# Performance work log

Measured on AMD Instinct MI355X. Metric: run time of the kernel, lower is better.

The kernel has to match this reference:

```python
import jax, jax.numpy as jnp
import numpy as np

N = 100000      # nodes
E = 1600000     # edges (before self-loops)
D = 14          # node_dim
H = 64          # hidden_dim
HEADS = 2
C = H // HEADS  # per-head channels = 32
NEG_SLOPE = 0.2 # GATv2Conv default


def setup_inputs() -> dict:
    key = jax.random.key(0)
    ks = jax.random.split(key, 32)
    p = lambda k, shape, s=0.05: (jax.random.normal(k, shape, jnp.float32) * s)
    inp = {
        'node_features': jax.random.normal(ks[0], (N, D), jnp.float32),
        'edge_index': jax.random.randint(ks[1], (2, E), 0, N, jnp.int32),
        # node_proj
        'proj_W': p(ks[2], (D, H)), 'proj_b': p(ks[3], (H,)),
        # GATv2 layer 1 (W_l for source msgs, W_r for target query)
        'g1_Wl': p(ks[4], (H, H)), 'g1_Wr': p(ks[5], (H, H)),
        'g1_att': p(ks[6], (HEADS, C)), 'g1_b': p(ks[7], (H,)),
        # GATv2 layer 2
        'g2_Wl': p(ks[8], (H, H)), 'g2_Wr': p(ks[9], (H, H)),
        'g2_att': p(ks[10], (HEADS, C)), 'g2_b': p(ks[11], (H,)),
        # LayerNorms
        'ln1_g': jnp.ones((H,), jnp.float32), 'ln1_b': jnp.zeros((H,), jnp.float32),
        'ln2_g': jnp.ones((H,), jnp.float32), 'ln2_b': jnp.zeros((H,), jnp.float32),
        # GRU (single step, h0=0). Gate order r,z,n like torch.
        'gru_Wi': p(ks[12], (H, 3 * H)), 'gru_Wh': p(ks[13], (H, 3 * H)),
        'gru_bi': p(ks[14], (3 * H,)), 'gru_bh': p(ks[15], (3 * H,)),
        # heads
        'hu_W': p(ks[16], (H, 1)), 'hu_b': p(ks[17], (1,)),
        'hf_W': p(ks[18], (H, 1)), 'hf_b': p(ks[19], (1,)),
        'ho_W': p(ks[20], (H, 1)), 'ho_b': p(ks[21], (1,)),
        'hc_W': p(ks[22], (H, 1)), 'hc_b': p(ks[23], (1,)),
    }
    return inp


def _layer_norm(x, g, b, eps=1e-5):
    mu = jnp.mean(x, axis=-1, keepdims=True)
    var = jnp.var(x, axis=-1, keepdims=True)
    return (x - mu) * jax.lax.rsqrt(var + eps) * g + b


def _gatv2(x, src, dst, Wl, Wr, att, b):
    n = x.shape[0]
    xl = (x @ Wl).reshape(n, HEADS, C)   # source messages
    xr = (x @ Wr).reshape(n, HEADS, C)   # target queries
    e = jax.nn.leaky_relu(xl[src] + xr[dst], NEG_SLOPE)       # [E', HEADS, C]
    s = jnp.einsum('ehc,hc->eh', e, att)                       # [E', HEADS]
    m = jax.ops.segment_max(s, dst, num_segments=n)            # segment softmax
    ex = jnp.exp(s - m[dst])
    den = jax.ops.segment_sum(ex, dst, num_segments=n)
    alpha = ex / (den[dst] + 1e-16)
    out = jax.ops.segment_sum(alpha[:, :, None] * xl[src], dst, num_segments=n)
    return out.reshape(n, H) + b


def reference(node_features, edge_index, proj_W, proj_b,
              g1_Wl, g1_Wr, g1_att, g1_b,
              g2_Wl, g2_Wr, g2_att, g2_b,
              ln1_g, ln1_b, ln2_g, ln2_b,
              gru_Wi, gru_Wh, gru_bi, gru_bh,
              hu_W, hu_b, hf_W, hf_b, ho_W, ho_b, hc_W, hc_b):
    n = node_features.shape[0]
    # add self-loops (PyG GATv2Conv default)
    loops = jnp.arange(n, dtype=edge_index.dtype)
    src = jnp.concatenate([edge_index[0], loops])
    dst = jnp.concatenate([edge_index[1], loops])

    x = node_features @ proj_W + proj_b
    x = jax.nn.elu(_gatv2(x, src, dst, g1_Wl, g1_Wr, g1_att, g1_b))
    x = _layer_norm(x, ln1_g, ln1_b)
    x = jax.nn.elu(_gatv2(x, src, dst, g2_Wl, g2_Wr, g2_att, g2_b))
    x = _layer_norm(x, ln2_g, ln2_b)

    # single-step GRU, h0 = 0 (gate order r, z, n as in torch)
    gi = x @ gru_Wi + gru_bi
    gi_r, gi_z, gi_n = jnp.split(gi, 3, axis=-1)
    bh_r, bh_z, bh_n = jnp.split(gru_bh, 3)
    r = jax.nn.sigmoid(gi_r + bh_r)
    z = jax.nn.sigmoid(gi_z + bh_z)
    nn_ = jnp.tanh(gi_n + r * bh_n)
    x = (1.0 - z) * nn_  # h' = (1-z)*n + z*h0, h0=0

    utilisation = jax.nn.sigmoid(x @ hu_W + hu_b)
    feasibility = jax.nn.sigmoid(x @ hf_W + hf_b)
    overtime = jax.nn.relu(x @ ho_W + ho_b)
    confidence = jax.nn.sigmoid(x @ hc_W + hc_b)
    return (utilisation, feasibility, overtime, confidence)
```

## Files before the change

### kernel.cpp

```cpp
#include <hip/hip_runtime.h>

#define NDIM 14
#define HDIM 64
#define NB 512
#define EPB 16
#define GSTR 72

typedef __attribute__((ext_vector_type(8))) _Float16 half8;
typedef __attribute__((ext_vector_type(2))) __fp16 fp16x2;
typedef __attribute__((ext_vector_type(4))) float f32x4;

static __device__ __forceinline__ float sigmoidf_(float x) { return 1.f / (1.f + __expf(-x)); }
static __device__ __forceinline__ float lrelu_(float x) { return x > 0.f ? x : 0.2f * x; }

static __device__ __forceinline__ float readlane_f(float x, int lane) {
  return __int_as_float(__builtin_amdgcn_readlane(__float_as_int(x), lane));
}

template <int CTRL>
static __device__ __forceinline__ float dpp_add_f(float x) {
  int v = __builtin_amdgcn_update_dpp(0, __float_as_int(x), CTRL, 0xF, 0xF, true);
  return x + __int_as_float(v);
}

static __device__ __forceinline__ float reduce16(float p) {
  p = dpp_add_f<0xB1>(p);
  p = dpp_add_f<0x4E>(p);
  p = dpp_add_f<0x141>(p);
  p = dpp_add_f<0x140>(p);
  return p;
}
static __device__ __forceinline__ float head_reduce32(float p) {
  p = reduce16(p);
  p += __int_as_float(__builtin_amdgcn_ds_swizzle(__float_as_int(p), 0x401F));
  return p;
}
static __device__ __forceinline__ float full_reduce64(float p) {
  p = head_reduce32(p);
  p += __shfl_xor(p, 32, 64);
  return p;
}

static __device__ __forceinline__ unsigned pk_add(unsigned a, unsigned b) {
  unsigned d; asm("v_pk_add_f16 %0, %1, %2" : "=v"(d) : "v"(a), "v"(b)); return d;
}
static __device__ __forceinline__ unsigned pk_mul(unsigned a, unsigned b) {
  unsigned d; asm("v_pk_mul_f16 %0, %1, %2" : "=v"(d) : "v"(a), "v"(b)); return d;
}
static __device__ __forceinline__ unsigned pk_max(unsigned a, unsigned b) {
  unsigned d; asm("v_pk_max_f16 %0, %1, %2" : "=v"(d) : "v"(a), "v"(b)); return d;
}
static __device__ __forceinline__ unsigned cvt_pk_u(float a, float b) {
  fp16x2 h = __builtin_amdgcn_cvt_pkrtz(a, b);
  unsigned u; __builtin_memcpy(&u, &h, 4); return u;
}
static __device__ __forceinline__ fp16x2 as_h2(unsigned u) {
  fp16x2 h; __builtin_memcpy(&h, &u, 4); return h;
}
static __device__ __forceinline__ float cvt_lo(unsigned u) {
  float r; asm("v_cvt_f32_f16 %0, %1" : "=v"(r) : "v"(u)); return r;
}
template <int CTRL>
static __device__ __forceinline__ unsigned pk_dpp_add(unsigned x) {
  unsigned v = (unsigned)__builtin_amdgcn_update_dpp(0, (int)x, CTRL, 0xF, 0xF, true);
  return pk_add(x, v);
}
static __device__ __forceinline__ unsigned pk_reduce32(unsigned p) {
  p = pk_dpp_add<0xB1>(p);
  p = pk_dpp_add<0x4E>(p);
  p = pk_dpp_add<0x141>(p);
  p = pk_dpp_add<0x140>(p);
  p = pk_add(p, (unsigned)__builtin_amdgcn_ds_swizzle((int)p, 0x401F));
  return p;
}

__global__ void k_binit(int* __restrict__ bcur, int cap) {
  int i = blockIdx.x * blockDim.x + threadIdx.x;
  if (i < NB) bcur[i] = i * cap;
}

__global__ void __launch_bounds__(256) k_bin(const int* __restrict__ ei,
                      long long* __restrict__ pairs, int* __restrict__ bucket_cur,
                      int E, int bsh) {
  __shared__ int h[NB];
  __shared__ int gb[NB];
  int t = threadIdx.x;
  for (int i = t; i < NB; i += 256) h[i] = 0;
  __syncthreads();
  int c0 = blockIdx.x * (256 * EPB);
  long long pr[EPB];
  int br[EPB];
#pragma unroll
  for (int i = 0; i < EPB; ++i) {
    int e = c0 + t + i * 256;
    if (e < E) {
      int s = ei[e], d = ei[E + e];
      int b = d >> bsh;
      int r = atomicAdd(&h[b], 1);
      pr[i] = ((long long)d << 32) | (unsigned)s;
      br[i] = b | (r << 9);
    } else br[i] = -1;
  }
  __syncthreads();
  for (int i = t; i < NB; i += 256)
    if (h[i]) gb[i] = atomicAdd(&bucket_cur[i], h[i]);
  __syncthreads();
#pragma unroll
  for (int i = 0; i < EPB; ++i) {
    if (br[i] >= 0) pairs[gb[br[i] & (NB - 1)] + (br[i] >> 9)] = pr[i];
  }
}

__global__ void __launch_bounds__(256) k_csr(const long long* __restrict__ pairs,
                      const int* __restrict__ bcur_final, int* __restrict__ row_off,
                      int* __restrict__ deg, int* __restrict__ csr_src,
                      int N, int bsh, int cap) {
  __shared__ int h[1024];
  __shared__ int cu[1024];
  __shared__ int wtot[4];
  int b = blockIdx.x;
  int node0 = b << bsh;
  int range = 1 << bsh;
  int nr = N - node0; if (nr > range) nr = range;
  if (nr <= 0) return;
  int e0 = b * cap, e1 = bcur_final[b];
  int tid = threadIdx.x;
  for (int i = tid; i < range; i += 256) h[i] = 0;
  __syncthreads();
  for (int e = e0 + tid; e < e1; e += 256)
    atomicAdd(&h[(int)(pairs[e] >> 32) - node0], 1);
  __syncthreads();
  if (range == 256) {
    int lane = tid & 63, wid = tid >> 6;
    int v = (tid < nr) ? h[tid] : 0;
    int x = v;
#pragma unroll
    for (int m = 1; m <= 32; m <<= 1) {
      int t2 = __shfl_up(x, m, 64);
      if (lane >= m) x += t2;
    }
    if (lane == 63) wtot[wid] = x;
    __syncthreads();
    int woff = 0;
#pragma unroll
    for (int w = 0; w < 4; ++w) woff += (w < wid) ? wtot[w] : 0;
    int excl = woff + x - v;
    if (tid < nr) {
      row_off[node0 + tid] = e0 + excl;
      deg[node0 + tid] = v;
      cu[tid] = excl;
    }
  } else {
    if (tid == 0) {
      int acc = 0;
      for (int i = 0; i < nr; ++i) {
        row_off[node0 + i] = e0 + acc;
        deg[node0 + i] = h[i];
        cu[i] = acc;
        acc += h[i];
      }
    }
  }
  __syncthreads();
  for (int e = e0 + tid; e < e1; e += 256) {
    long long pk = pairs[e];
    int d = (int)(pk >> 32), s = (int)pk;
    int p = atomicAdd(&cu[d - node0], 1);
    csr_src[e0 + p] = s;
  }
}

__global__ void k_wprep(const float* __restrict__ projW, const float* __restrict__ projB,
                        const float* __restrict__ Wl1, const float* __restrict__ Wr1,
                        const float* __restrict__ Wi, const float* __restrict__ Wl2,
                        const float* __restrict__ Wr2,
                        float* __restrict__ Wfl, float* __restrict__ Wfr,
                        float* __restrict__ bfl, float* __restrict__ bfr,
                        _Float16* __restrict__ Wt, _Float16* __restrict__ Wb) {
  int blk = blockIdx.x;
  if (blk < 4) {
    int t = blk * 256 + threadIdx.x;
    int total = (NDIM + 1) * HDIM;
    if (t >= total) return;
    int r = t / HDIM, c = t % HDIM;
    float al = 0.f, ar = 0.f;
    if (r < NDIM) {
      for (int k = 0; k < HDIM; ++k) {
        float w = projW[r * HDIM + k];
        al += w * Wl1[k * HDIM + c];
        ar += w * Wr1[k * HDIM + c];
      }
      Wfl[r * HDIM + c] = al;
      Wfr[r * HDIM + c] = ar;
    } else {
      for (int k = 0; k < HDIM; ++k) {
        float w = projB[k];
        al += w * Wl1[k * HDIM + c];
        ar += w * Wr1[k * HDIM + c];
      }
      bfl[c] = al;
      bfr[c] = ar;
    }
  } else if (blk < 52) {
    int t = (blk - 4) * 256 + threadIdx.x;
    if (t >= 192 * 64) return;
    int col = t / 64, row = t % 64;
    Wt[col * GSTR + row] = (_Float16)Wi[row * 192 + col];
  } else {
    int t = (blk - 52) * 256 + threadIdx.x;
    if (t >= 128 * 64) return;
    int col = t >> 6, row = t & 63;
    float v = (col < 64) ? Wl2[row * 64 + col] : Wr2[row * 64 + (col - 64)];
    Wb[col * GSTR + row] = (_Float16)v;
  }
}

__global__ void k1_xlxr(const float* __restrict__ nf, const float* __restrict__ Wfl,
                        const float* __restrict__ Wfr, const float* __restrict__ bfl,
                        const float* __restrict__ bfr, _Float16* __restrict__ XL16,
                        float* __restrict__ XR, int N) {
  int n = blockIdx.x * (blockDim.x >> 6) + (threadIdx.x >> 6);
  int j = threadIdx.x & 63;
  if (n >= N) return;
  float nfv = (j < NDIM) ? nf[n * NDIM + j] : 0.f;
  float al = bfl[j], ar = bfr[j];
#pragma unroll
  for (int k = 0; k < NDIM; ++k) {
    float xk = readlane_f(nfv, k);
    al += xk * Wfl[k * HDIM + j];
    ar += xk * Wfr[k * HDIM + j];
  }
  XL16[n * HDIM + j] = (_Float16)al;
  XR[n * HDIM + j] = ar;
}

__global__ void k_agg(const int* __restrict__ csr_src, const int* __restrict__ row_off,
                      const int* __restrict__ deg, const _Float16* __restrict__ XL16,
                      const float* __restrict__ XR, const float* __restrict__ att,
                      const float* __restrict__ gb, const float* __restrict__ lng,
                      const float* __restrict__ lnb, float* __restrict__ Y, int N) {
  int n = blockIdx.x * (blockDim.x >> 6) + (threadIdx.x >> 6);
  int j = threadIdx.x & 63;
  if (n >= N) return;
  float xr = XR[n * HDIM + j];
  float attv = att[j];
  unsigned xr_pk  = cvt_pk_u(xr, xr);
  unsigned att_pk = cvt_pk_u(attv, attv);
  unsigned c02_pk = 0x32663266u;
  fp16x2 one_pk = as_h2(0x3C003C00u);
  const unsigned short* XLu = (const unsigned short*)XL16;
  unsigned ju = (unsigned)j;

  float xl = (float)XL16[(size_t)n * HDIM + j];
  float p = head_reduce32(lrelu_(xl + xr) * attv);
  float ex = __expf(p);
  float acc0 = ex * xl, acc1 = 0.f;
  float den0 = ex, den1 = 0.f;

  int base = row_off[n], cnt = deg[n];
  for (int c0 = 0; c0 < cnt; c0 += 64) {
    int m_ = cnt - c0; if (m_ > 64) m_ = 64;
    int sidx = (j < m_) ? csr_src[base + c0 + j] : 0;
    int npairs = m_ >> 1;
    int pp = 0;
    for (; pp + 8 <= npairs; pp += 8) {
      unsigned x[8];
#pragma unroll
      for (int u = 0; u < 8; ++u) {
        int sa = __builtin_amdgcn_readlane(sidx, 2 * (pp + u));
        int sb = __builtin_amdgcn_readlane(sidx, 2 * (pp + u) + 1);
        unsigned short ua = XLu[((unsigned)sa << 6) + ju];
        unsigned short ub = XLu[((unsigned)sb << 6) + ju];
        x[u] = (unsigned)ua | ((unsigned)ub << 16);
      }
#pragma unroll
      for (int u = 0; u < 8; ++u) {
        unsigned t = pk_add(x[u], xr_pk);
        unsigned lr = pk_max(t, pk_mul(t, c02_pk));
        unsigned sc = pk_mul(lr, att_pk);
        sc = pk_reduce32(sc);
        float s_a = cvt_lo(sc), s_b = cvt_lo(sc >> 16);
        float e_a = __expf(s_a), e_b = __expf(s_b);
        fp16x2 exk = __builtin_amdgcn_cvt_pkrtz(e_a, e_b);
        if (u & 1) {
          acc1 = __builtin_amdgcn_fdot2(as_h2(x[u]), exk, acc1, false);
          den1 = __builtin_amdgcn_fdot2(exk, one_pk, den1, false);
        } else {
          acc0 = __builtin_amdgcn_fdot2(as_h2(x[u]), exk, acc0, false);
          den0 = __builtin_amdgcn_fdot2(exk, one_pk, den0, false);
        }
      }
    }
    for (; pp < npairs; ++pp) {
      int sa = __builtin_amdgcn_readlane(sidx, 2 * pp);
      int sb = __builtin_amdgcn_readlane(sidx, 2 * pp + 1);
      unsigned short ua = XLu[((unsigned)sa << 6) + ju];
      unsigned short ub = XLu[((unsigned)sb << 6) + ju];
      unsigned xu = (unsigned)ua | ((unsigned)ub << 16);
      unsigned t = pk_add(xu, xr_pk);
      unsigned lr = pk_max(t, pk_mul(t, c02_pk));
      unsigned sc = pk_mul(lr, att_pk);
      sc = pk_reduce32(sc);
      float s_a = cvt_lo(sc), s_b = cvt_lo(sc >> 16);
      float e_a = __expf(s_a), e_b = __expf(s_b);
      fp16x2 exk = __builtin_amdgcn_cvt_pkrtz(e_a, e_b);
      acc0 = __builtin_amdgcn_fdot2(as_h2(xu), exk, acc0, false);
      den0 = __builtin_amdgcn_fdot2(exk, one_pk, den0, false);
    }
    if (m_ & 1) {
      int s = __builtin_amdgcn_readlane(sidx, m_ - 1);
      float xls = (float)XL16[(size_t)s * HDIM + j];
      float pq = head_reduce32(lrelu_(xls + xr) * attv);
      float ee = __expf(pq);
      acc0 += ee * xls;
      den0 += ee;
    }
  }

  float acc = acc0 + acc1;
  float den = den0 + den1;
  float y = acc / (den + 1e-16f) + gb[j];
  y = y > 0.f ? y : __expf(y) - 1.f;
  float mu = full_reduce64(y) * (1.f / 64.f);
  float d = y - mu;
  float var = full_reduce64(d * d) * (1.f / 64.f);
  Y[n * HDIM + j] = d * rsqrtf(var + 1e-5f) * lng[j] + lnb[j];
}

__global__ void __launch_bounds__(256) k3_mfma(const float* __restrict__ Y,
                      const _Float16* __restrict__ Wb, _Float16* __restrict__ XL16,
                      float* __restrict__ XR, int N) {
  __shared__ _Float16 W[128 * GSTR];
  for (int i = threadIdx.x; i < 128 * GSTR / 8; i += 256)
    ((int4*)W)[i] = ((const int4*)Wb)[i];
  __syncthreads();
  int wave = blockIdx.x * 4 + (threadIdx.x >> 6);
  int nwaves = gridDim.x * 4;
  int lane = threadIdx.x & 63;
  int c = lane & 15, q = lane >> 4;
  for (int n0 = wave * 16; n0 < N; n0 += nwaves * 16) {
    bool okrow = (n0 + c) < N;
    const float* yrow = Y + (size_t)(n0 + c) * HDIM + q * 8;
    float4 v0 = {0,0,0,0}, v1 = {0,0,0,0}, v2 = {0,0,0,0}, v3 = {0,0,0,0};
    if (okrow) {
      v0 = *(const float4*)(yrow);
      v1 = *(const float4*)(yrow + 4);
      v2 = *(const float4*)(yrow + 32);
      v3 = *(const float4*)(yrow + 36);
    }
    half8 a0, a1;
    a0[0]=(_Float16)v0.x; a0[1]=(_Float16)v0.y; a0[2]=(_Float16)v0.z; a0[3]=(_Float16)v0.w;
    a0[4]=(_Float16)v1.x; a0[5]=(_Float16)v1.y; a0[6]=(_Float16)v1.z; a0[7]=(_Float16)v1.w;
    a1[0]=(_Float16)v2.x; a1[1]=(_Float16)v2.y; a1[2]=(_Float16)v2.z; a1[3]=(_Float16)v2.w;
    a1[4]=(_Float16)v3.x; a1[5]=(_Float16)v3.y; a1[6]=(_Float16)v3.z; a1[7]=(_Float16)v3.w;

    f32x4 acc[8];
#pragma unroll
    for (int t = 0; t < 8; ++t) acc[t] = (f32x4){0.f, 0.f, 0.f, 0.f};
#pragma unroll
    for (int t = 0; t < 8; ++t) {
      half8 b0 = *(const half8*)(&W[(t * 16 + c) * GSTR + q * 8]);
      half8 b1 = *(const half8*)(&W[(t * 16 + c) * GSTR + 32 + q * 8]);
      acc[t] = __builtin_amdgcn_mfma_f32_16x16x32_f16(a0, b0, acc[t], 0, 0, 0);
      acc[t] = __builtin_amdgcn_mfma_f32_16x16x32_f16(a1, b1, acc[t], 0, 0, 0);
    }
#pragma unroll
    for (int t = 0; t < 4; ++t) {
#pragma unroll
      for (int i = 0; i < 4; ++i) {
        int n = n0 + q * 4 + i;
        if (n < N) {
          XL16[(size_t)n * HDIM + t * 16 + c] = (_Float16)acc[t][i];
          XR[(size_t)n * HDIM + t * 16 + c] = acc[t + 4][i];
        }
      }
    }
  }
}

__global__ void __launch_bounds__(256) k5_gru_mfma(const float* __restrict__ Y,
                       const _Float16* __restrict__ Wt,
                       const float* __restrict__ bi, const float* __restrict__ bh,
                       const float* __restrict__ huW, const float* __restrict__ hub,
                       const float* __restrict__ hfW, const float* __restrict__ hfb,
                       const float* __restrict__ hoW, const float* __restrict__ hob,
                       const float* __restrict__ hcW, const float* __restrict__ hcb,
                       float* __restrict__ out, int N) {
  __shared__ _Float16 W[192 * GSTR];
  __shared__ float BS[192];
  __shared__ float BHN[64];
  for (int i = threadIdx.x; i < 192 * GSTR / 8; i += 256)
    ((int4*)W)[i] = ((const int4*)Wt)[i];
  for (int i = threadIdx.x; i < 192; i += 256) BS[i] = bi[i] + (i < 128 ? bh[i] : 0.f);
  for (int i = threadIdx.x; i < 64; i += 256) BHN[i] = bh[128 + i];
  __syncthreads();

  int wave = blockIdx.x * 4 + (threadIdx.x >> 6);
  int nwaves = gridDim.x * 4;
  int lane = threadIdx.x & 63;
  int c = lane & 15, q = lane >> 4;

  float hu_[4], hf_[4], ho_[4], hc_[4];
#pragma unroll
  for (int t = 0; t < 4; ++t) {
    hu_[t] = huW[t * 16 + c];
    hf_[t] = hfW[t * 16 + c];
    ho_[t] = hoW[t * 16 + c];
    hc_[t] = hcW[t * 16 + c];
  }
  float hub0 = hub[0], hfb0 = hfb[0], hob0 = hob[0], hcb0 = hcb[0];

  for (int n0 = wave * 16; n0 < N; n0 += nwaves * 16) {
    bool okrow = (n0 + c) < N;
    const float* yrow = Y + (size_t)(n0 + c) * HDIM + q * 8;
    float4 v0 = {0,0,0,0}, v1 = {0,0,0,0}, v2 = {0,0,0,0}, v3 = {0,0,0,0};
    if (okrow) {
      v0 = *(const float4*)(yrow);
      v1 = *(const float4*)(yrow + 4);
      v2 = *(const float4*)(yrow + 32);
      v3 = *(const float4*)(yrow + 36);
    }
    half8 a0, a1;
    a0[0]=(_Float16)v0.x; a0[1]=(_Float16)v0.y; a0[2]=(_Float16)v0.z; a0[3]=(_Float16)v0.w;
    a0[4]=(_Float16)v1.x; a0[5]=(_Float16)v1.y; a0[6]=(_Float16)v1.z; a0[7]=(_Float16)v1.w;
    a1[0]=(_Float16)v2.x; a1[1]=(_Float16)v2.y; a1[2]=(_Float16)v2.z; a1[3]=(_Float16)v2.w;
    a1[4]=(_Float16)v3.x; a1[5]=(_Float16)v3.y; a1[6]=(_Float16)v3.z; a1[7]=(_Float16)v3.w;

    f32x4 acc[12];
#pragma unroll
    for (int t = 0; t < 12; ++t) acc[t] = (f32x4){0.f, 0.f, 0.f, 0.f};
#pragma unroll
    for (int t = 0; t < 12; ++t) {
      half8 b0 = *(const half8*)(&W[(t * 16 + c) * GSTR + q * 8]);
      half8 b1 = *(const half8*)(&W[(t * 16 + c) * GSTR + 32 + q * 8]);
      acc[t] = __builtin_amdgcn_mfma_f32_16x16x32_f16(a0, b0, acc[t], 0, 0, 0);
      acc[t] = __builtin_amdgcn_mfma_f32_16x16x32_f16(a1, b1, acc[t], 0, 0, 0);
    }

    float hv[4][4];
#pragma unroll
    for (int t = 0; t < 4; ++t) {
      int cr = t * 16 + c;
      float bsr = BS[cr], bsz = BS[64 + cr], bsn = BS[128 + cr], bhn = BHN[cr];
#pragma unroll
      for (int i = 0; i < 4; ++i) {
        float r = sigmoidf_(acc[t][i] + bsr);
        float z = sigmoidf_(acc[t + 4][i] + bsz);
        float nn = tanhf(acc[t + 8][i] + bsn + r * bhn);
        hv[t][i] = (1.f - z) * nn;
      }
    }
#pragma unroll
    for (int i = 0; i < 4; ++i) {
      float pu = 0.f, pf = 0.f, po = 0.f, pc = 0.f;
#pragma unroll
      for (int t = 0; t < 4; ++t) {
        pu += hv[t][i] * hu_[t];
        pf += hv[t][i] * hf_[t];
        po += hv[t][i] * ho_[t];
        pc += hv[t][i] * hc_[t];
      }
      pu = reduce16(pu); pf = reduce16(pf); po = reduce16(po); pc = reduce16(pc);
      int n = n0 + q * 4 + i;
      if (n < N) {
        if (c == 0) out[n]         = sigmoidf_(pu + hub0);
        if (c == 1) out[N + n]     = sigmoidf_(pf + hfb0);
        if (c == 2) out[2 * N + n] = fmaxf(po + hob0, 0.f);
        if (c == 3) out[3 * N + n] = sigmoidf_(pc + hcb0);
      }
    }
  }
}

extern "C" void kernel_launch(void* const* d_in, const int* in_sizes, int n_in,
                              void* d_out, int out_size, void* d_ws, size_t ws_size,
                              hipStream_t stream) {
  const float* nf    = (const float*)d_in[0];
  const int*   ei    = (const int*)d_in[1];
  const float* projW = (const float*)d_in[2];
  const float* projB = (const float*)d_in[3];
  const float* g1Wl  = (const float*)d_in[4];
  const float* g1Wr  = (const float*)d_in[5];
  const float* g1att = (const float*)d_in[6];
  const float* g1b   = (const float*)d_in[7];
  const float* g2Wl  = (const float*)d_in[8];
  const float* g2Wr  = (const float*)d_in[9];
  const float* g2att = (const float*)d_in[10];
  const float* g2b   = (const float*)d_in[11];
  const float* ln1g  = (const float*)d_in[12];
  const float* ln1b  = (const float*)d_in[13];
  const float* ln2g  = (const float*)d_in[14];
  const float* ln2b  = (const float*)d_in[15];
  const float* gruWi = (const float*)d_in[16];
  const float* gruBi = (const float*)d_in[18];
  const float* gruBh = (const float*)d_in[19];
  const float* huW = (const float*)d_in[20];
  const float* hub = (const float*)d_in[21];
  const float* hfW = (const float*)d_in[22];
  const float* hfb = (const float*)d_in[23];
  const float* hoW = (const float*)d_in[24];
  const float* hob = (const float*)d_in[25];
  const float* hcW = (const float*)d_in[26];
  const float* hcb = (const float*)d_in[27];
  float* out = (float*)d_out;

  const int N = in_sizes[0] / NDIM;
  const int E = in_sizes[1] / 2;
  int bsh = 8;
  while (((N - 1) >> bsh) >= NB) ++bsh;
  const int nbu = (N + (1 << bsh) - 1) >> bsh;
  const int cap = (E + nbu - 1) / nbu + 768;

  char* ws = (char*)d_ws;
  size_t off = 0;
  auto carve = [&](size_t bytes) { void* p = ws + off; off += (bytes + 255) & ~size_t(255); return p; };
  _Float16*  XL16    = (_Float16*)carve(sizeof(_Float16) * N * HDIM);
  float*     XR      = (float*)carve(sizeof(float) * N * HDIM);
  float*     Y       = (float*)carve(sizeof(float) * N * HDIM);
  long long* pairs   = (long long*)carve(sizeof(long long) * (size_t)nbu * cap);
  int*       csr_src = (int*)carve(sizeof(int) * (size_t)nbu * cap);
  int*       deg     = (int*)carve(sizeof(int) * N);
  int*       row_off = (int*)carve(sizeof(int) * N);
  int*       bcur    = (int*)carve(sizeof(int) * NB);
  float*     Wfl     = (float*)carve(sizeof(float) * NDIM * HDIM);
  float*     Wfr     = (float*)carve(sizeof(float) * NDIM * HDIM);
  float*     bfl     = (float*)carve(sizeof(float) * HDIM);
  float*     bfr     = (float*)carve(sizeof(float) * HDIM);
  _Float16*  Wt      = (_Float16*)carve(sizeof(_Float16) * 192 * GSTR);
  _Float16*  Wb      = (_Float16*)carve(sizeof(_Float16) * 128 * GSTR);

  const int BLK = 256;
  dim3 b(BLK);
  dim3 gridWaveN((N + 3) / 4);
  dim3 gridBin((E + BLK * EPB - 1) / (BLK * EPB));

  k_binit<<<dim3(2), b, 0, stream>>>(bcur, cap);
  k_bin<<<gridBin, b, 0, stream>>>(ei, pairs, bcur, E, bsh);
  k_csr<<<dim3(nbu), b, 0, stream>>>(pairs, bcur, row_off, deg, csr_src, N, bsh, cap);

  k_wprep<<<dim3(84), b, 0, stream>>>(projW, projB, g1Wl, g1Wr, gruWi, g2Wl, g2Wr,
                                      Wfl, Wfr, bfl, bfr, Wt, Wb);

  k1_xlxr<<<gridWaveN, b, 0, stream>>>(nf, Wfl, Wfr, bfl, bfr, XL16, XR, N);
  k_agg<<<gridWaveN, b, 0, stream>>>(csr_src, row_off, deg, XL16, XR, g1att, g1b, ln1g, ln1b, Y, N);
  k3_mfma<<<dim3(800), b, 0, stream>>>(Y, Wb, XL16, XR, N);
  k_agg<<<gridWaveN, b, 0, stream>>>(csr_src, row_off, deg, XL16, XR, g2att, g2b, ln2g, ln2b, Y, N);
  k5_gru_mfma<<<dim3(800), b, 0, stream>>>(Y, Wt, gruBi, gruBh,
                                           huW, hub, hfW, hfb, hoW, hob, hcW, hcb, out, N);
}
```

Before: 366.2 us.

## Process two destination nodes per wave in GAT aggregation, interleaving gathers

The aggregation kernel now assigns two destination nodes to each wave and interleaves their 8-pair gather groups, so one node's XL loads are in flight while the other's scores are computed. The odd-tail path is replaced by masking exponentials to zero inside padded groups, and the pair-packing uses a perm instruction. The bucket-cursor init kernel is folded into the weight-prep kernel, removing one launch. The interleaving costs more registers and can cut occupancy, and nodes with very different degrees leave part of the wave's work serialized.

```diff
diff --git a/kernel.cpp b/kernel.cpp
--- a/kernel.cpp
+++ b/kernel.cpp
@@ -72,11 +72,6 @@
   p = pk_dpp_add<0x140>(p);
   p = pk_add(p, (unsigned)__builtin_amdgcn_ds_swizzle((int)p, 0x401F));
   return p;
-}
-
-__global__ void k_binit(int* __restrict__ bcur, int cap) {
-  int i = blockIdx.x * blockDim.x + threadIdx.x;
-  if (i < NB) bcur[i] = i * cap;
 }
 
 __global__ void __launch_bounds__(256) k_bin(const int* __restrict__ ei,
@@ -176,7 +171,8 @@
                         const float* __restrict__ Wr2,
                         float* __restrict__ Wfl, float* __restrict__ Wfr,
                         float* __restrict__ bfl, float* __restrict__ bfr,
-                        _Float16* __restrict__ Wt, _Float16* __restrict__ Wb) {
+                        _Float16* __restrict__ Wt, _Float16* __restrict__ Wb,
+                        int* __restrict__ bcur, int cap) {
   int blk = blockIdx.x;
   if (blk < 4) {
     int t = blk * 256 + threadIdx.x;
@@ -206,12 +202,15 @@
     if (t >= 192 * 64) return;
     int col = t / 64, row = t % 64;
     Wt[col * GSTR + row] = (_Float16)Wi[row * 192 + col];
-  } else {
+  } else if (blk < 84) {
     int t = (blk - 52) * 256 + threadIdx.x;
     if (t >= 128 * 64) return;
     int col = t >> 6, row = t & 63;
     float v = (col < 64) ? Wl2[row * 64 + col] : Wr2[row * 64 + (col - 64)];
     Wb[col * GSTR + row] = (_Float16)v;
+  } else {
+    int i = (blk - 84) * 256 + threadIdx.x;
+    if (i < NB) bcur[i] = i * cap;
   }
 }
 
@@ -234,97 +233,129 @@
   XR[n * HDIM + j] = ar;
 }
 
+#define LOAD8G(xb_, sidx_, g_)                                   \
+  _Pragma("unroll") for (int u = 0; u < 8; ++u) {                \
+    int pi_ = (g_) * 8 + u;                                      \
+    int sa_ = __builtin_amdgcn_readlane(sidx_, 2 * pi_);         \
+    int sb_ = __builtin_amdgcn_readlane(sidx_, 2 * pi_ + 1);     \
+    unsigned ua_ = XLu[((unsigned)sa_ << 6) + ju];               \
+    unsigned ub_ = XLu[((unsigned)sb_ << 6) + ju];               \
+    xb_[u] = __builtin_amdgcn_perm(ub_, ua_, 0x05040100u);       \
+  }
+
+#define PROC8G(xb_, g_, m_, xrpk_, a0_, a1_, d0_, d1_)           \
+  _Pragma("unroll") for (int u = 0; u < 8; ++u) {                \
+    int pi_ = (g_) * 8 + u;                                      \
+    unsigned t_ = pk_add(xb_[u], xrpk_);                         \
+    unsigned lr_ = pk_max(t_, pk_mul(t_, c02_pk));               \
+    unsigned sc_ = pk_mul(lr_, att_pk);                          \
+    sc_ = pk_reduce32(sc_);                                      \
+    float sfa_ = cvt_lo(sc_), sfb_ = cvt_lo(sc_ >> 16);          \
+    float ea_ = __expf(sfa_), eb_ = __expf(sfb_);                \
+    ea_ = (2 * pi_ < (m_)) ? ea_ : 0.f;                          \
+    eb_ = (2 * pi_ + 1 < (m_)) ? eb_ : 0.f;                      \
+    fp16x2 exk_ = __builtin_amdgcn_cvt_pkrtz(ea_, eb_);          \
+    if (u & 1) {                                                 \
+      a1_ = __builtin_amdgcn_fdot2(as_h2(xb_[u]), exk_, a1_, false); \
+      d1_ = __builtin_amdgcn_fdot2(exk_, one_pk, d1_, false);    \
+    } else {                                                     \
+      a0_ = __builtin_amdgcn_fdot2(as_h2(xb_[u]), exk_, a0_, false); \
+      d0_ = __builtin_amdgcn_fdot2(exk_, one_pk, d0_, false);    \
+    }                                                            \
+  }
+
 __global__ void k_agg(const int* __restrict__ csr_src, const int* __restrict__ row_off,
                       const int* __restrict__ deg, const _Float16* __restrict__ XL16,
                       const float* __restrict__ XR, const float* __restrict__ att,
                       const float* __restrict__ gb, const float* __restrict__ lng,
                       const float* __restrict__ lnb, float* __restrict__ Y, int N) {
-  int n = blockIdx.x * (blockDim.x >> 6) + (threadIdx.x >> 6);
+  int wid = blockIdx.x * (blockDim.x >> 6) + (threadIdx.x >> 6);
   int j = threadIdx.x & 63;
-  if (n >= N) return;
-  float xr = XR[n * HDIM + j];
+  int nA = wid * 2;
+  if (nA >= N) return;
+  int nB = nA + 1;
+  bool hasB = nB < N;
+  int nBc = hasB ? nB : nA;
+
   float attv = att[j];
-  unsigned xr_pk  = cvt_pk_u(xr, xr);
   unsigned att_pk = cvt_pk_u(attv, attv);
   unsigned c02_pk = 0x32663266u;
   fp16x2 one_pk = as_h2(0x3C003C00u);
   const unsigned short* XLu = (const unsigned short*)XL16;
   unsigned ju = (unsigned)j;
 
-  float xl = (float)XL16[(size_t)n * HDIM + j];
-  float p = head_reduce32(lrelu_(xl + xr) * attv);
-  float ex = __expf(p);
-  float acc0 = ex * xl, acc1 = 0.f;
-  float den0 = ex, den1 = 0.f;
-
-  int base = row_off[n], cnt = deg[n];
-  for (int c0 = 0; c0 < cnt; c0 += 64) {
-    int m_ = cnt - c0; if (m_ > 64) m_ = 64;
-    int sidx = (j < m_) ? csr_src[base + c0 + j] : 0;
-    int npairs = m_ >> 1;
-    int pp = 0;
-    for (; pp + 8 <= npairs; pp += 8) {
-      unsigned x[8];
-#pragma unroll
-      for (int u = 0; u < 8; ++u) {
-        int sa = __builtin_amdgcn_readlane(sidx, 2 * (pp + u));
-        int sb = __builtin_amdgcn_readlane(sidx, 2 * (pp + u) + 1);
-        unsigned short ua = XLu[((unsigned)sa << 6) + ju];
-        unsigned short ub = XLu[((unsigned)sb << 6) + ju];
-        x[u] = (unsigned)ua | ((unsigned)ub << 16);
-      }
-#pragma unroll
-      for (int u = 0; u < 8; ++u) {
-        unsigned t = pk_add(x[u], xr_pk);
-        unsigned lr = pk_max(t, pk_mul(t, c02_pk));
-        unsigned sc = pk_mul(lr, att_pk);
-        sc = pk_reduce32(sc);
-        float s_a = cvt_lo(sc), s_b = cvt_lo(sc >> 16);
-        float e_a = __expf(s_a), e_b = __expf(s_b);
-        fp16x2 exk = __builtin_amdgcn_cvt_pkrtz(e_a, e_b);
-        if (u & 1) {
-          acc1 = __builtin_amdgcn_fdot2(as_h2(x[u]), exk, acc1, false);
-          den1 = __builtin_amdgcn_fdot2(exk, one_pk, den1, false);
-        } else {
-          acc0 = __builtin_amdgcn_fdot2(as_h2(x[u]), exk, acc0, false);
-          den0 = __builtin_amdgcn_fdot2(exk, one_pk, den0, false);
-        }
-      }
-    }
-    for (; pp < npairs; ++pp) {
-      int sa = __builtin_amdgcn_readlane(sidx, 2 * pp);
-      int sb = __builtin_amdgcn_readlane(sidx, 2 * pp + 1);
-      unsigned short ua = XLu[((unsigned)sa << 6) + ju];
-      unsigned short ub = XLu[((unsigned)sb << 6) + ju];
-      unsigned xu = (unsigned)ua | ((unsigned)ub << 16);
-      unsigned t = pk_add(xu, xr_pk);
-      unsigned lr = pk_max(t, pk_mul(t, c02_pk));
-      unsigned sc = pk_mul(lr, att_pk);
-      sc = pk_reduce32(sc);
-      float s_a = cvt_lo(sc), s_b = cvt_lo(sc >> 16);
-      float e_a = __expf(s_a), e_b = __expf(s_b);
-      fp16x2 exk = __builtin_amdgcn_cvt_pkrtz(e_a, e_b);
-      acc0 = __builtin_amdgcn_fdot2(as_h2(xu), exk, acc0, false);
-      den0 = __builtin_amdgcn_fdot2(exk, one_pk, den0, false);
-    }
-    if (m_ & 1) {
-      int s = __builtin_amdgcn_readlane(sidx, m_ - 1);
-      float xls = (float)XL16[(size_t)s * HDIM + j];
-      float pq = head_reduce32(lrelu_(xls + xr) * attv);
-      float ee = __expf(pq);
-      acc0 += ee * xls;
-      den0 += ee;
-    }
-  }
-
-  float acc = acc0 + acc1;
-  float den = den0 + den1;
-  float y = acc / (den + 1e-16f) + gb[j];
-  y = y > 0.f ? y : __expf(y) - 1.f;
-  float mu = full_reduce64(y) * (1.f / 64.f);
-  float d = y - mu;
-  float var = full_reduce64(d * d) * (1.f / 64.f);
-  Y[n * HDIM + j] = d * rsqrtf(var + 1e-5f) * lng[j] + lnb[j];
+  float xrA = XR[(size_t)nA * HDIM + j];
+  float xrB = XR[(size_t)nBc * HDIM + j];
+  unsigned xr_pkA = cvt_pk_u(xrA, xrA);
+  unsigned xr_pkB = cvt_pk_u(xrB, xrB);
+
+  float xlA = (float)XL16[(size_t)nA * HDIM + j];
+  float pA = head_reduce32(lrelu_(xlA + xrA) * attv);
+  float exA = __expf(pA);
+  float aA0 = exA * xlA, aA1 = 0.f, dA0 = exA, dA1 = 0.f;
+
+  float xlB = (float)XL16[(size_t)nBc * HDIM + j];
+  float pB = head_reduce32(lrelu_(xlB + xrB) * attv);
+  float exB = __expf(pB);
+  float aB0 = exB * xlB, aB1 = 0.f, dB0 = exB, dB1 = 0.f;
+
+  int baseA = row_off[nA], cntA = deg[nA];
+  int baseB = hasB ? row_off[nB] : 0;
+  int cntB = hasB ? deg[nB] : 0;
+  int mA = cntA < 64 ? cntA : 64;
+  int mB = cntB < 64 ? cntB : 64;
+  int sidxA = (j < mA) ? csr_src[baseA + j] : 0;
+  int sidxB = (j < mB) ? csr_src[baseB + j] : 0;
+  int ngA = (((mA + 1) >> 1) + 7) >> 3;
+  int ngB = (((mB + 1) >> 1) + 7) >> 3;
+
+  unsigned xa[8], xb[8];
+  int gA = 0, gB = 0;
+  while (gA < ngA || gB < ngB) {
+    bool doA = gA < ngA, doB = gB < ngB;
+    if (doA) { LOAD8G(xa, sidxA, gA); }
+    if (doB) { LOAD8G(xb, sidxB, gB); }
+    if (doA) { PROC8G(xa, gA, mA, xr_pkA, aA0, aA1, dA0, dA1); ++gA; }
+    if (doB) { PROC8G(xb, gB, mB, xr_pkB, aB0, aB1, dB0, dB1); ++gB; }
+  }
+
+  for (int c0 = 64; c0 < cntA; c0 += 64) {
+    int m_ = cntA - c0; if (m_ > 64) m_ = 64;
+    int sidx = (j < m_) ? csr_src[baseA + c0 + j] : 0;
+    int ng = (((m_ + 1) >> 1) + 7) >> 3;
+    for (int g = 0; g < ng; ++g) {
+      LOAD8G(xa, sidx, g);
+      PROC8G(xa, g, m_, xr_pkA, aA0, aA1, dA0, dA1);
+    }
+  }
+  for (int c0 = 64; c0 < cntB; c0 += 64) {
+    int m_ = cntB - c0; if (m_ > 64) m_ = 64;
+    int sidx = (j < m_) ? csr_src[baseB + c0 + j] : 0;
+    int ng = (((m_ + 1) >> 1) + 7) >> 3;
+    for (int g = 0; g < ng; ++g) {
+      LOAD8G(xb, sidx, g);
+      PROC8G(xb, g, m_, xr_pkB, aB0, aB1, dB0, dB1);
+    }
+  }
+
+  {
+    float acc = aA0 + aA1, den = dA0 + dA1;
+    float y = acc / (den + 1e-16f) + gb[j];
+    y = y > 0.f ? y : __expf(y) - 1.f;
+    float mu = full_reduce64(y) * (1.f / 64.f);
+    float d = y - mu;
+    float var = full_reduce64(d * d) * (1.f / 64.f);
+    Y[(size_t)nA * HDIM + j] = d * rsqrtf(var + 1e-5f) * lng[j] + lnb[j];
+  }
+  if (hasB) {
+    float acc = aB0 + aB1, den = dB0 + dB1;
+    float y = acc / (den + 1e-16f) + gb[j];
+    y = y > 0.f ? y : __expf(y) - 1.f;
+    float mu = full_reduce64(y) * (1.f / 64.f);
+    float d = y - mu;
+    float var = full_reduce64(d * d) * (1.f / 64.f);
+    Y[(size_t)nB * HDIM + j] = d * rsqrtf(var + 1e-5f) * lng[j] + lnb[j];
+  }
 }
 
 __global__ void __launch_bounds__(256) k3_mfma(const float* __restrict__ Y,
@@ -532,19 +563,19 @@
   const int BLK = 256;
   dim3 b(BLK);
   dim3 gridWaveN((N + 3) / 4);
+  dim3 gridAgg(((N + 1) / 2 + 3) / 4);
   dim3 gridBin((E + BLK * EPB - 1) / (BLK * EPB));
 
-  k_binit<<<dim3(2), b, 0, stream>>>(bcur, cap);
+  k_wprep<<<dim3(86), b, 0, stream>>>(projW, projB, g1Wl, g1Wr, gruWi, g2Wl, g2Wr,
+                                      Wfl, Wfr, bfl, bfr, Wt, Wb, bcur, cap);
+
   k_bin<<<gridBin, b, 0, stream>>>(ei, pairs, bcur, E, bsh);
   k_csr<<<dim3(nbu), b, 0, stream>>>(pairs, bcur, row_off, deg, csr_src, N, bsh, cap);
 
-  k_wprep<<<dim3(84), b, 0, stream>>>(projW, projB, g1Wl, g1Wr, gruWi, g2Wl, g2Wr,
-                                      Wfl, Wfr, bfl, bfr, Wt, Wb);
-
   k1_xlxr<<<gridWaveN, b, 0, stream>>>(nf, Wfl, Wfr, bfl, bfr, XL16, XR, N);
-  k_agg<<<gridWaveN, b, 0, stream>>>(csr_src, row_off, deg, XL16, XR, g1att, g1b, ln1g, ln1b, Y, N);
+  k_agg<<<gridAgg, b, 0, stream>>>(csr_src, row_off, deg, XL16, XR, g1att, g1b, ln1g, ln1b, Y, N);
   k3_mfma<<<dim3(800), b, 0, stream>>>(Y, Wb, XL16, XR, N);
-  k_agg<<<gridWaveN, b, 0, stream>>>(csr_src, row_off, deg, XL16, XR, g2att, g2b, ln2g, ln2b, Y, N);
+  k_agg<<<gridAgg, b, 0, stream>>>(csr_src, row_off, deg, XL16, XR, g2att, g2b, ln2g, ln2b, Y, N);
   k5_gru_mfma<<<dim3(800), b, 0, stream>>>(Y, Wt, gruBi, gruBh,
                                            huW, hub, hfW, hfb, hoW, hob, hcW, hcb, out, N);
 }
```

After: 422.1 us. 1.15x slower.
